# Performance work log

Hardware: AMD Instinct MI355X
Metric: run time of the kernel (lower is better)

## Reference

```python
import jax, jax.numpy as jnp
import numpy as np

DIM_LIST = [8, 8, 8, 8, 8, 8, 8, 8]
RANK_LIST = [1, 64, 64, 64, 64, 64, 64, 64, 1]
ORDER = 4                      # tensor_input_order
PADDED_IN = int(np.prod(DIM_LIST[:ORDER]))   # 4096
NUM_OUT = int(np.prod(DIM_LIST[ORDER:]))     # 4096
BATCH = 8192
NUM_IN = 4000                  # < PADDED_IN, exercises padding path


def setup_inputs() -> dict:
    key = jax.random.key(0)
    keys = jax.random.split(key, 10)
    x = jax.random.normal(keys[0], (BATCH, NUM_IN), dtype=jnp.float32)
    cores = {}
    for i in range(8):
        shp = (RANK_LIST[i], DIM_LIST[i], RANK_LIST[i + 1])
        cores[f"c{i}"] = 0.1 * jax.random.normal(keys[1 + i], shp, dtype=jnp.float32)
    bias = jax.random.normal(keys[9], (NUM_OUT,), dtype=jnp.float32)
    return {"x": x, **cores, "bias": bias}


def _tt_forward(x, cores, bias):
    B = x.shape[0]
    pad = PADDED_IN - x.shape[-1]
    xp = jnp.pad(x, ((0, 0), (0, pad))) if pad > 0 else x
    # ---- contract input modes with first ORDER cores ----
    z = xp.reshape(B, DIM_LIST[0], -1)            # (B, d0, M)
    z = jnp.einsum('bdm,dr->bmr', z, cores[0][0])  # core0 has r0=1
    for i in range(1, ORDER):
        d = DIM_LIST[i]
        Bz, M, r = z.shape
        z = z.reshape(B, d, M // d, r)
        z = jnp.einsum('bdmr,rds->bms', z, cores[i])
    # z: (B, 1, r_k)
    y = z
    # ---- expand output modes with remaining cores ----
    for i in range(ORDER, len(DIM_LIST)):
        y = jnp.einsum('bpr,rds->bpds', y, cores[i])
        y = y.reshape(B, -1, cores[i].shape[-1])
    out = y.reshape(B, -1)[:, :NUM_OUT]
    return out + bias


def reference(x, c0, c1, c2, c3, c4, c5, c6, c7, bias):
    cores = [c0, c1, c2, c3, c4, c5, c6, c7]
    return _tt_forward(x, cores, bias)
```

## Files before the change

kernel.cpp:

```cpp
#include <hip/hip_runtime.h>
#include <hip/hip_bf16.h>


typedef __attribute__((ext_vector_type(8))) short short8;
typedef __attribute__((ext_vector_type(4))) short s16x4;
typedef __attribute__((ext_vector_type(4))) float f32x4;

__device__ __forceinline__ short f2bf(float f) {
    union { float f; unsigned u; } c; c.f = f;
    unsigned u = c.u;
    unsigned r = (u + 0x7fffu + ((u >> 16) & 1u)) >> 16;
    return (short)r;
}

__global__ __launch_bounds__(256) void tt_chain_fused(
    const float* __restrict__ c0, const float* __restrict__ c1,
    const float* __restrict__ c2, const float* __restrict__ c3,
    const float* __restrict__ c4, const float* __restrict__ c5,
    const float* __restrict__ c6, const float* __restrict__ c7,
    short* __restrict__ A4f, short* __restrict__ B4f) {
    __shared__ float sm[1024];
    const int t = threadIdx.x;
    if (blockIdx.x < 1024) {
        const int bid = blockIdx.x;
        const int i = bid >> 1;
        const int a2r = bid >> 4;
        float* A2r_ = sm;
        float* A3r_ = sm + 64;
        if (t < 64) {
            const int i1 = a2r >> 3, d1 = a2r & 7;
            float acc = 0.f;
            for (int r = 0; r < 64; ++r)
                acc += c0[i1 * 64 + r] * c1[(r * 8 + d1) * 64 + t];
            A2r_[t] = acc;
        }
        __syncthreads();
        if (t < 64) {
            const int d2 = i & 7;
            float acc = 0.f;
            for (int r = 0; r < 64; ++r)
                acc += A2r_[r] * c2[(r * 8 + d2) * 64 + t];
            A3r_[t] = acc;
        }
        __syncthreads();
        {
            const int kk = t >> 6, s = t & 63;
            const int k = (bid << 2) + kk, d3 = k & 7;
            float acc = 0.f;
            for (int r = 0; r < 64; ++r)
                acc += A3r_[r] * c3[(r * 8 + d3) * 64 + s];
            A4f[(((k >> 5) * 4 + (s >> 4)) << 9) + (((k >> 3) & 3) << 7) +
                ((s & 15) << 3) + (k & 7)] = f2bf(acc);
        }
    } else {
        const int cb = blockIdx.x - 1024;
        const int d4 = cb & 7, jgrp = cb >> 3;
        const int d5 = jgrp >> 3;
        const int d6 = jgrp & 7;
        float* B6l = sm;
        float* B5l = sm + 512;
        for (int o = t; o < 512; o += 256) {
            const int q6 = o >> 3, jj = o & 7;
            float acc = 0.f;
            for (int q7 = 0; q7 < 64; ++q7)
                acc += c6[(q6 * 8 + d6) * 64 + q7] * c7[q7 * 8 + jj];
            B6l[o] = acc;
        }
        __syncthreads();
        for (int o = t; o < 512; o += 256) {
            const int q5 = o >> 3, jj = o & 7;
            float acc = 0.f;
            for (int q6 = 0; q6 < 64; ++q6)
                acc += c5[(q5 * 8 + d5) * 64 + q6] * B6l[q6 * 8 + jj];
            B5l[o] = acc;
        }
        __syncthreads();
        for (int o = t; o < 512; o += 256) {
            const int nl = o >> 6, r4 = o & 63;
            float acc = 0.f;
            for (int q5 = 0; q5 < 64; ++q5)
                acc += c4[(r4 * 8 + d4) * 64 + q5] * B5l[q5 * 8 + nl];
            const int n = d4 * 512 + jgrp * 8 + nl;
            B4f[(((n >> 4) * 2 + (r4 >> 5)) << 9) + (((r4 >> 3) & 3) << 7) +
                ((n & 15) << 3) + (r4 & 7)] = f2bf(acc);
        }
    }
}

__global__ __launch_bounds__(1024, 8) void fused_gemm_v2(
    const float* __restrict__ x, const short* __restrict__ A4f,
    const short* __restrict__ B4f, const float* __restrict__ bias,
    float* __restrict__ out) {
    __shared__ __align__(16) char smem[51200];
    float* zsm  = (float*)smem;
    short* Bs   = (short*)smem;
    float* slab = (float*)(smem + 32768);
    short* zbl  = (short*)(smem + 49152);
    const int tid = threadIdx.x, wave = tid >> 6, lane = tid & 63;
    const int m0 = blockIdx.x << 4;
    const int r16 = lane & 15, hi = lane >> 4, kq = hi << 3;

    const float* xp = x + (long)(m0 + r16) * 4000 + kq;
    const short* a4p = A4f + (lane << 3);
    {
        f32x4 acc[4] = {};
#pragma unroll 2
        for (int t = wave; t < 125; t += 16) {
            const int k0 = t << 5;
            f32x4 u0 = *(const f32x4*)(xp + k0);
            f32x4 u1 = *(const f32x4*)(xp + k0 + 4);
            short8 a;
            a[0] = f2bf(u0[0]); a[1] = f2bf(u0[1]);
            a[2] = f2bf(u0[2]); a[3] = f2bf(u0[3]);
            a[4] = f2bf(u1[0]); a[5] = f2bf(u1[1]);
            a[6] = f2bf(u1[2]); a[7] = f2bf(u1[3]);
#pragma unroll
            for (int f = 0; f < 4; ++f) {
                short8 b = *(const short8*)(a4p + (((t << 2) + f) << 9));
                acc[f] = __builtin_amdgcn_mfma_f32_16x16x32_bf16(a, b, acc[f], 0, 0, 0);
            }
        }
        const int prow = hi << 2;
        if (wave < 8) {
#pragma unroll
            for (int f = 0; f < 4; ++f)
#pragma unroll
                for (int u = 0; u < 4; ++u)
                    zsm[wave * 1024 + (prow + u) * 64 + f * 16 + r16] = acc[f][u];
        }
        __syncthreads();
        if (wave >= 8) {
            float* zs = zsm + (wave - 8) * 1024;
#pragma unroll
            for (int f = 0; f < 4; ++f)
#pragma unroll
                for (int u = 0; u < 4; ++u)
                    zs[(prow + u) * 64 + f * 16 + r16] += acc[f][u];
        }
        __syncthreads();
    }
    if (tid < 256) {
        const f32x4* zp = (const f32x4*)zsm;
        f32x4 s = zp[tid];
#pragma unroll
        for (int w = 1; w < 8; ++w) s += zp[w * 256 + tid];
        s16x4 o;
#pragma unroll
        for (int u = 0; u < 4; ++u) o[u] = f2bf(s[u]);
        *(s16x4*)(zbl + (tid >> 4) * 64 + ((tid & 15) << 2)) = o;
    }
    __syncthreads();

    const short8 az0 = *(const short8*)(zbl + r16 * 64 + kq);
    const short8 az1 = *(const short8*)(zbl + r16 * 64 + 32 + kq);
    const long orow = (long)(m0 + (lane >> 2)) * 4096;
    for (int c = 0; c < 16; ++c) {
        const short* src0 = B4f + c * 16384 + wave * 512 + (lane << 3);
        __builtin_amdgcn_global_load_lds(
            (const __attribute__((address_space(1))) void*)src0,
            (__attribute__((address_space(3))) void*)(Bs + wave * 512), 16, 0, 0);
        __builtin_amdgcn_global_load_lds(
            (const __attribute__((address_space(1))) void*)(src0 + 8192),
            (__attribute__((address_space(3))) void*)(Bs + 8192 + wave * 512), 16, 0, 0);
        __syncthreads();
        const short8 b0 = *(const short8*)(Bs + (wave * 2) * 512 + (lane << 3));
        const short8 b1 = *(const short8*)(Bs + (wave * 2 + 1) * 512 + (lane << 3));
        f32x4 a = {};
        a = __builtin_amdgcn_mfma_f32_16x16x32_bf16(az0, b0, a, 0, 0, 0);
        a = __builtin_amdgcn_mfma_f32_16x16x32_bf16(az1, b1, a, 0, 0, 0);
        float* sl = slab + wave * 256;
#pragma unroll
        for (int u = 0; u < 4; ++u)
            sl[(((hi << 2) + u) << 4) + r16] = a[u];
        __syncthreads();
        f32x4 v = *(const f32x4*)(sl + ((lane >> 2) << 4) + ((lane & 3) << 2));
        const int ncol = c * 256 + wave * 16 + ((lane & 3) << 2);
        v += *(const f32x4*)(bias + ncol);
        *(f32x4*)(out + orow + ncol) = v;
    }
}

extern "C" void kernel_launch(void* const* d_in, const int* in_sizes, int n_in,
                              void* d_out, int out_size, void* d_ws, size_t ws_size,
                              hipStream_t stream) {
    const float* x    = (const float*)d_in[0];
    const float* c0   = (const float*)d_in[1];
    const float* c1   = (const float*)d_in[2];
    const float* c2   = (const float*)d_in[3];
    const float* c3   = (const float*)d_in[4];
    const float* c4   = (const float*)d_in[5];
    const float* c5   = (const float*)d_in[6];
    const float* c6   = (const float*)d_in[7];
    const float* c7   = (const float*)d_in[8];
    const float* bias = (const float*)d_in[9];
    float* out = (float*)d_out;

    char* ws = (char*)d_ws;
    short* A4f = (short*)ws;
    short* B4f = (short*)(ws + (512u << 10));

    tt_chain_fused<<<1536, 256, 0, stream>>>(c0, c1, c2, c3, c4, c5, c6, c7,
                                             A4f, B4f);
    fused_gemm_v2<<<512, 1024, 0, stream>>>(x, A4f, B4f, bias, out);
}
```

Before: 98.64 us.

## Drop LDS staging and barriers in output GEMM; write results directly

The second GEMM stage now loads B fragments straight from global memory instead of staging them through LDS with global_load_lds. Each wave writes its MFMA outputs directly to global memory with bias added, so the per-iteration slab transpose and both barriers go away. The first-stage reduction now stores all 16 wave partials into a larger LDS buffer and sums them in one pass, replacing the two-phase add. The trade-offs are narrower, less coalesced output stores (16 floats per row segment per instruction), a 64KB+ LDS footprint that may limit occupancy, and more redundant global reads of B.

```diff
diff --git a/kernel.cpp b/kernel.cpp
--- a/kernel.cpp
+++ b/kernel.cpp
@@ -87,22 +87,19 @@
     }
 }
 
-__global__ __launch_bounds__(1024, 8) void fused_gemm_v2(
+__global__ __launch_bounds__(1024, 8) void tt_gemm_fused(
     const float* __restrict__ x, const short* __restrict__ A4f,
     const short* __restrict__ B4f, const float* __restrict__ bias,
     float* __restrict__ out) {
-    __shared__ __align__(16) char smem[51200];
-    float* zsm  = (float*)smem;
-    short* Bs   = (short*)smem;
-    float* slab = (float*)(smem + 32768);
-    short* zbl  = (short*)(smem + 49152);
+    __shared__ float zsm[16 * 1024];
+    __shared__ short zbl[16 * 64];
     const int tid = threadIdx.x, wave = tid >> 6, lane = tid & 63;
     const int m0 = blockIdx.x << 4;
     const int r16 = lane & 15, hi = lane >> 4, kq = hi << 3;
 
-    const float* xp = x + (long)(m0 + r16) * 4000 + kq;
-    const short* a4p = A4f + (lane << 3);
     {
+        const float* xp = x + (long)(m0 + r16) * 4000 + kq;
+        const short* a4p = A4f + (lane << 3);
         f32x4 acc[4] = {};
 #pragma unroll 2
         for (int t = wave; t < 125; t += 16) {
@@ -121,29 +118,18 @@
             }
         }
         const int prow = hi << 2;
-        if (wave < 8) {
 #pragma unroll
-            for (int f = 0; f < 4; ++f)
+        for (int f = 0; f < 4; ++f)
 #pragma unroll
-                for (int u = 0; u < 4; ++u)
-                    zsm[wave * 1024 + (prow + u) * 64 + f * 16 + r16] = acc[f][u];
-        }
-        __syncthreads();
-        if (wave >= 8) {
-            float* zs = zsm + (wave - 8) * 1024;
-#pragma unroll
-            for (int f = 0; f < 4; ++f)
-#pragma unroll
-                for (int u = 0; u < 4; ++u)
-                    zs[(prow + u) * 64 + f * 16 + r16] += acc[f][u];
-        }
-        __syncthreads();
+            for (int u = 0; u < 4; ++u)
+                zsm[wave * 1024 + (prow + u) * 64 + f * 16 + r16] = acc[f][u];
     }
+    __syncthreads();
     if (tid < 256) {
         const f32x4* zp = (const f32x4*)zsm;
         f32x4 s = zp[tid];
 #pragma unroll
-        for (int w = 1; w < 8; ++w) s += zp[w * 256 + tid];
+        for (int w = 1; w < 16; ++w) s += zp[w * 256 + tid];
         s16x4 o;
 #pragma unroll
         for (int u = 0; u < 4; ++u) o[u] = f2bf(s[u]);
@@ -153,30 +139,20 @@
 
     const short8 az0 = *(const short8*)(zbl + r16 * 64 + kq);
     const short8 az1 = *(const short8*)(zbl + r16 * 64 + 32 + kq);
-    const long orow = (long)(m0 + (lane >> 2)) * 4096;
+#pragma unroll 4
     for (int c = 0; c < 16; ++c) {
-        const short* src0 = B4f + c * 16384 + wave * 512 + (lane << 3);
-        __builtin_amdgcn_global_load_lds(
-            (const __attribute__((address_space(1))) void*)src0,
-            (__attribute__((address_space(3))) void*)(Bs + wave * 512), 16, 0, 0);
-        __builtin_amdgcn_global_load_lds(
-            (const __attribute__((address_space(1))) void*)(src0 + 8192),
-            (__attribute__((address_space(3))) void*)(Bs + 8192 + wave * 512), 16, 0, 0);
-        __syncthreads();
-        const short8 b0 = *(const short8*)(Bs + (wave * 2) * 512 + (lane << 3));
-        const short8 b1 = *(const short8*)(Bs + (wave * 2 + 1) * 512 + (lane << 3));
+        const int fi = (wave << 4) + c;
+        const short* bp = B4f + (fi << 10) + (lane << 3);
+        const short8 b0 = *(const short8*)(bp);
+        const short8 b1 = *(const short8*)(bp + 512);
         f32x4 a = {};
         a = __builtin_amdgcn_mfma_f32_16x16x32_bf16(az0, b0, a, 0, 0, 0);
         a = __builtin_amdgcn_mfma_f32_16x16x32_bf16(az1, b1, a, 0, 0, 0);
-        float* sl = slab + wave * 256;
+        const int ncol = (fi << 4) + r16;
+        const float bz = bias[ncol];
 #pragma unroll
         for (int u = 0; u < 4; ++u)
-            sl[(((hi << 2) + u) << 4) + r16] = a[u];
-        __syncthreads();
-        f32x4 v = *(const f32x4*)(sl + ((lane >> 2) << 4) + ((lane & 3) << 2));
-        const int ncol = c * 256 + wave * 16 + ((lane & 3) << 2);
-        v += *(const f32x4*)(bias + ncol);
-        *(f32x4*)(out + orow + ncol) = v;
+            out[(long)(m0 + (hi << 2) + u) * 4096 + ncol] = a[u] + bz;
     }
 }
 
@@ -201,5 +177,5 @@
 
     tt_chain_fused<<<1536, 256, 0, stream>>>(c0, c1, c2, c3, c4, c5, c6, c7,
                                              A4f, B4f);
-    fused_gemm_v2<<<512, 1024, 0, stream>>>(x, A4f, B4f, bias, out);
+    tt_gemm_fused<<<512, 1024, 0, stream>>>(x, A4f, B4f, bias, out);
 }
```

New measurement: 97.90 us. Within noise of the previous version (-0.7%).
